# Optimization experiments

Hardware: AMD Instinct MI355X
Metric: run time of the kernel (lower is better)

The kernel has to match this reference:

```python
import jax, jax.numpy as jnp
import numpy as np

B, IN, OUT, LAT = 8192, 256, 256, 128

def setup_inputs() -> dict:
    key = jax.random.key(0)
    ks = jax.random.split(key, 6)
    s = 0.05
    return {
        "x": jax.random.normal(ks[0], (B, IN), dtype=jnp.float32),
        "latent": jax.random.normal(ks[1], (B, LAT), dtype=jnp.float32),
        "Ww": jax.random.normal(ks[2], (LAT, IN * OUT), dtype=jnp.float32) * s,
        "bw": jax.random.normal(ks[3], (IN * OUT,), dtype=jnp.float32) * s,
        "Wb": jax.random.normal(ks[4], (LAT, OUT), dtype=jnp.float32) * s,
        "bb": jax.random.normal(ks[5], (OUT,), dtype=jnp.float32) * s,
    }

def reference(x, latent, Ww, bw, Wb, bb):
    lead = x.shape[:-1]
    x2 = x.reshape(-1, x.shape[-1])            # [B, in]
    l2 = latent.reshape(-1, latent.shape[-1])  # [B, lat]
    # per-sample weight: [B, in, out]
    weight = (l2 @ Ww + bw).reshape(-1, IN, OUT)
    # per-sample bias: [B, out]
    bias = l2 @ Wb + bb
    out = jnp.einsum('bi,bio->bo', x2, weight) + bias
    return out.reshape(*lead, OUT)
```

## Files before the change

### kernel.cpp

```cpp
#include <hip/hip_runtime.h>
#include <cstdint>
#include <cstddef>

#define BATCH  8192
#define IN_N   256
#define OUT_N  256
#define LAT_N  128
#define SLABS  129
#define KT     (SLABS * IN_N)
#define KT16   (KT / 16)
#define SPLITK 4

typedef _Float16 h8 __attribute__((ext_vector_type(8)));
typedef _Float16 h4 __attribute__((ext_vector_type(4)));
typedef _Float16 h2 __attribute__((ext_vector_type(2)));
typedef float    f16v __attribute__((ext_vector_type(16)));
typedef float    f4v  __attribute__((ext_vector_type(4)));

#define AS1 __attribute__((address_space(1)))
#define AS3 __attribute__((address_space(3)))
#define WAITVM0 asm volatile("s_waitcnt vmcnt(0)" ::: "memory")
#define WAITVM2 asm volatile("s_waitcnt vmcnt(2)" ::: "memory")
#define WAITVM3 asm volatile("s_waitcnt vmcnt(3)" ::: "memory")

#define WS_BP    0
#define WS_XH    16908288
#define WS_LT    21102592
#define WS_PARTS 23216128

#define PR_T1   516
#define PR_L1   580
#define PR_X1   1604
#define PR_O1   1608
#define PR_B1   2632
__global__ void k_prep(const float* __restrict__ Ww, const float* __restrict__ bw,
                       const float* __restrict__ x,  const float* __restrict__ latent,
                       const float* __restrict__ Wb, const float* __restrict__ bb,
                       _Float16* __restrict__ Bp, _Float16* __restrict__ Xh,
                       _Float16* __restrict__ LT, float* __restrict__ part0) {
    __shared__ _Float16 smemh[16512];
    const int bid = blockIdx.x;
    const int t   = threadIdx.x;

    if (bid < PR_T1) {
        _Float16* tile = smemh;
        const int k0 = bid * 64;
#pragma unroll
        for (int j = 0; j < 16; ++j) {
            int idx = j * 256 + t;
            int row = idx >> 6, col = (idx & 63) * 4;
            int k = k0 + row;
            const float* src = (k < LAT_N * IN_N)
                             ? Ww + (size_t)k * 256 + col
                             : bw + (size_t)(k - LAT_N * IN_N) * 256 + col;
            float4 v = *(const float4*)src;
            h4 o;
            o[0] = (_Float16)v.x; o[1] = (_Float16)v.y;
            o[2] = (_Float16)v.z; o[3] = (_Float16)v.w;
            *(h4*)(tile + row * 256 + col) = o;
        }
        __syncthreads();
        const int tl = t & 31;
#pragma unroll
        for (int j = 0; j < 4; ++j) {
            int stid = j * 8 + (t >> 5);
            int kt_l = stid >> 3, nt = stid & 7;
            int kt16 = bid * 4 + kt_l;
            _Float16* dst = Bp + ((size_t)(nt * KT16 + kt16) * 64) * 8;
#pragma unroll
            for (int kh = 0; kh < 2; ++kh) {
                h8 v;
#pragma unroll
                for (int h = 0; h < 8; ++h)
                    v[h] = tile[(kt_l * 16 + kh * 8 + h) * 256 + nt * 32 + tl];
                *(h8*)(dst + (size_t)(kh * 32 + tl) * 8) = v;
            }
        }
    } else if (bid < PR_L1) {
        _Float16* t2 = smemh;
        const int b0 = (bid - PR_T1) * 128;
#pragma unroll
        for (int j = 0; j < 16; ++j) {
            int idx = j * 256 + t;
            int b = idx >> 5, l = (idx & 31) * 4;
            float4 v = *(const float4*)(latent + (size_t)(b0 + b) * 128 + l);
            t2[(l + 0) * 129 + b] = (_Float16)v.x;
            t2[(l + 1) * 129 + b] = (_Float16)v.y;
            t2[(l + 2) * 129 + b] = (_Float16)v.z;
            t2[(l + 3) * 129 + b] = (_Float16)v.w;
        }
        __syncthreads();
#pragma unroll
        for (int j = 0; j < 32; ++j) {
            int idx = j * 256 + t;
            int l = idx >> 6, bb2 = (idx & 63) * 2;
            h2 w;
            w[0] = t2[l * 129 + bb2];
            w[1] = t2[l * 129 + bb2 + 1];
            *(h2*)(LT + (size_t)l * BATCH + b0 + bb2) = w;
        }
    } else if (bid < PR_X1) {
        const int cb = bid - PR_L1;
        int i = (cb * 256 + t) * 8;
        float4 v0 = *(const float4*)(x + i);
        float4 v1 = *(const float4*)(x + i + 4);
        h8 o;
        o[0] = (_Float16)v0.x; o[1] = (_Float16)v0.y;
        o[2] = (_Float16)v0.z; o[3] = (_Float16)v0.w;
        o[4] = (_Float16)v1.x; o[5] = (_Float16)v1.y;
        o[6] = (_Float16)v1.z; o[7] = (_Float16)v1.w;
        *(h8*)(Xh + i) = o;
    } else if (bid < PR_O1) {
        const int ob = bid - PR_X1;
        int base = ob * 2048 + t * 8;
        h8 o;
#pragma unroll
        for (int h = 0; h < 8; ++h) o[h] = (_Float16)1.0f;
        *(h8*)(LT + (size_t)LAT_N * BATCH + base) = o;
    } else {
        float* lat = (float*)smemh;
        const int b0 = (bid - PR_O1) * 8;
#pragma unroll
        for (int j = 0; j < 4; ++j) {
            int idx = t + 256 * j;
            int rr = idx >> 7, l = idx & 127;
            lat[rr * 128 + l] = latent[(size_t)(b0 + rr) * 128 + l];
        }
        __syncthreads();
        const int o = t;
        float acc[8];
        float bbv = bb[o];
#pragma unroll
        for (int rr = 0; rr < 8; ++rr) acc[rr] = bbv;
        for (int l = 0; l < 128; ++l) {
            float w = Wb[l * 256 + o];
#pragma unroll
            for (int rr = 0; rr < 8; ++rr) acc[rr] += lat[rr * 128 + l] * w;
        }
#pragma unroll
        for (int rr = 0; rr < 8; ++rr) part0[(size_t)(b0 + rr) * 256 + o] = acc[rr];
    }
}

__global__ __launch_bounds__(512, 2) void k_gemm(const _Float16* __restrict__ Bp,
                                                 const _Float16* __restrict__ Xh,
                                                 const _Float16* __restrict__ LT,
                                                 float* __restrict__ parts) {
    __shared__ __align__(16) _Float16 Bs[4 * 8192];

    const int bid   = blockIdx.x;
    const int ks    = bid & 3;
    const int m_blk = bid >> 2;
    const int m0    = m_blk * 128;
    const int slab0 = (ks == 0) ? 0 : 33 + 32 * (ks - 1);
    const int nslab = (ks == 0) ? 33 : 32;

    const int tid = threadIdx.x, wid = tid >> 6, lane = tid & 63;
    const int l32 = lane & 31, khalf = lane >> 5;
    const int wm = wid >> 1, wn = wid & 1;
    const int wn4 = wn * 4;
    const int mrow = m0 + wm * 32 + l32;

    h8 xv[16];
    const _Float16* xp = Xh + (size_t)mrow * IN_N + khalf * 8;
#pragma unroll
    for (int k = 0; k < 16; ++k) xv[k] = *(const h8*)(xp + k * 16);

    const _Float16* ltp = LT + (size_t)slab0 * BATCH;
    _Float16 s_cur = ltp[mrow];

    const int chunk0 = wid * 2;
    const int ktl0 = chunk0 >> 3, nt0 = chunk0 & 7;
    const char* Bgb = (const char*)Bp;

#define STAGE(bufidx, ktg)                                                                 \
    do {                                                                                   \
        const char* g0_ = Bgb + (((size_t)(nt0 * KT16 + (ktg) + ktl0)) << 10) + (lane << 4);     \
        const char* g1_ = Bgb + (((size_t)((nt0 + 1) * KT16 + (ktg) + ktl0)) << 10) + (lane << 4); \
        _Float16* l0_ = Bs + (bufidx) * 8192 + chunk0 * 512;                               \
        __builtin_amdgcn_global_load_lds((const AS1 void*)g0_, (AS3 void*)l0_, 16, 0, 0);  \
        __builtin_amdgcn_global_load_lds((const AS1 void*)g1_, (AS3 void*)(l0_ + 512), 16, 0, 0); \
    } while (0)

    f16v acc0, acc1, acc2, acc3;
#pragma unroll
    for (int r = 0; r < 16; ++r) { acc0[r] = 0.f; acc1[r] = 0.f; acc2[r] = 0.f; acc3[r] = 0.f; }

#define KSTEP(bufc, sl)                                                                    \
    _Pragma("unroll")                                                                      \
    for (int j = 0; j < 2; ++j) {                                                          \
        const int kx = (((sl) * 2 + j) & 15);                                              \
        h8 a = xv[kx] * s8;                                                                \
        const _Float16* bb = Bs + (bufc) * 8192 + j * 4096 + wn4 * 512 + (lane << 3);      \
        h8 b0 = *(const h8*)(bb);                                                          \
        h8 b1 = *(const h8*)(bb + 512);                                                    \
        h8 b2 = *(const h8*)(bb + 1024);                                                   \
        h8 b3 = *(const h8*)(bb + 1536);                                                   \
        acc0 = __builtin_amdgcn_mfma_f32_32x32x16_f16(a, b0, acc0, 0, 0, 0);               \
        acc1 = __builtin_amdgcn_mfma_f32_32x32x16_f16(a, b1, acc1, 0, 0, 0);               \
        acc2 = __builtin_amdgcn_mfma_f32_32x32x16_f16(a, b2, acc2, 0, 0, 0);               \
        acc3 = __builtin_amdgcn_mfma_f32_32x32x16_f16(a, b3, acc3, 0, 0, 0);               \
    }

    const int kb = slab0 * 16;

    STAGE(0, kb + 0);
    STAGE(1, kb + 2);
    WAITVM2;
    __builtin_amdgcn_s_barrier();
    asm volatile("" ::: "memory");

    for (int s0 = 0; s0 < nslab - 1; ++s0) {
        _Float16 s_nx = ltp[(size_t)(s0 + 1) * BATCH + mrow];
        h8 s8;
#pragma unroll
        for (int h = 0; h < 8; ++h) s8[h] = s_cur;
        const int ktg0 = kb + s0 * 16;
#pragma unroll
        for (int sl = 0; sl < 8; ++sl) {
            STAGE((sl + 2) & 3, ktg0 + (sl + 2) * 2);
            KSTEP(sl & 3, sl);
            if (sl == 0) WAITVM3; else WAITVM2;
            __builtin_amdgcn_s_barrier();
            asm volatile("" ::: "memory");
        }
        s_cur = s_nx;
    }

    {
        h8 s8;
#pragma unroll
        for (int h = 0; h < 8; ++h) s8[h] = s_cur;
        const int ktg0 = kb + (nslab - 1) * 16;
#pragma unroll
        for (int sl = 0; sl < 8; ++sl) {
            if (sl < 6) STAGE((sl + 2) & 3, ktg0 + (sl + 2) * 2);
            KSTEP(sl & 3, sl);
            if (sl < 7) {
                if (sl == 6) WAITVM0; else WAITVM2;
                __builtin_amdgcn_s_barrier();
                asm volatile("" ::: "memory");
            }
        }
    }

    float* dst = parts + (size_t)ks * ((size_t)BATCH * OUT_N);
    const int rowb = m0 + wm * 32;
#define EPI(u, accv)                                                                       \
    {                                                                                      \
        int col = wn * 128 + (u) * 32 + l32;                                               \
        _Pragma("unroll")                                                                  \
        for (int r = 0; r < 16; ++r) {                                                     \
            int row = rowb + (r & 3) + 8 * (r >> 2) + 4 * khalf;                           \
            size_t off = (size_t)row * OUT_N + col;                                        \
            if (ks == 0) dst[off] += accv[r];                                              \
            else         dst[off] = accv[r];                                               \
        }                                                                                  \
    }
    EPI(0, acc0); EPI(1, acc1); EPI(2, acc2); EPI(3, acc3);
#undef EPI
#undef KSTEP
#undef STAGE
}

__global__ void k_reduce(const float* __restrict__ parts, float* __restrict__ out) {
    int i = (blockIdx.x * 256 + threadIdx.x) * 4;
    f4v s = *(const f4v*)(parts + i);
    s += *(const f4v*)(parts + 2097152 + i);
    s += *(const f4v*)(parts + 2 * 2097152 + i);
    s += *(const f4v*)(parts + 3 * 2097152 + i);
    *(f4v*)(out + i) = s;
}

extern "C" void kernel_launch(void* const* d_in, const int* in_sizes, int n_in,
                              void* d_out, int out_size, void* d_ws, size_t ws_size,
                              hipStream_t stream) {
    const float* x      = (const float*)d_in[0];
    const float* latent = (const float*)d_in[1];
    const float* Ww     = (const float*)d_in[2];
    const float* bw     = (const float*)d_in[3];
    const float* Wb     = (const float*)d_in[4];
    const float* bb     = (const float*)d_in[5];

    char* ws = (char*)d_ws;
    _Float16* Bp    = (_Float16*)(ws + WS_BP);
    _Float16* Xh    = (_Float16*)(ws + WS_XH);
    _Float16* LT    = (_Float16*)(ws + WS_LT);
    float*    parts = (float*)(ws + WS_PARTS);
    float*    out   = (float*)d_out;

    k_prep<<<PR_B1, 256, 0, stream>>>(Ww, bw, x, latent, Wb, bb, Bp, Xh, LT, parts);
    k_gemm<<<256, 512, 0, stream>>>(Bp, Xh, LT, parts);
    k_reduce<<<2048, 256, 0, stream>>>(parts, out);
}
```

Before: 252.2 us.

## Retile GEMM warps to 64x64 sub-tiles and drop occupancy hint to one

Changes the per-warp tile from 32 rows x 128 columns to 64 rows x 64 columns (2x2 MFMA blocks). Each warp now loads two B fragments from LDS instead of four per k-step, halving LDS read traffic per MFMA, but it keeps two rows of X in registers (32 h8 vectors) and scales two A operands. Launch bounds drop to one block per CU to make room for the added registers, and the wait count at slab start is adjusted for the extra latent load. The risk is lost occupancy and less latency hiding.

Result: slower. 267.2 us (+6.0%).

```diff
diff --git a/kernel.cpp b/kernel.cpp
--- a/kernel.cpp
+++ b/kernel.cpp
@@ -21,7 +21,7 @@
 #define AS3 __attribute__((address_space(3)))
 #define WAITVM0 asm volatile("s_waitcnt vmcnt(0)" ::: "memory")
 #define WAITVM2 asm volatile("s_waitcnt vmcnt(2)" ::: "memory")
-#define WAITVM3 asm volatile("s_waitcnt vmcnt(3)" ::: "memory")
+#define WAITVM4 asm volatile("s_waitcnt vmcnt(4)" ::: "memory")
 
 #define WS_BP    0
 #define WS_XH    16908288
@@ -142,7 +142,7 @@
     }
 }
 
-__global__ __launch_bounds__(512, 2) void k_gemm(const _Float16* __restrict__ Bp,
+__global__ __launch_bounds__(512, 1) void k_gemm(const _Float16* __restrict__ Bp,
                                                  const _Float16* __restrict__ Xh,
                                                  const _Float16* __restrict__ LT,
                                                  float* __restrict__ parts) {
@@ -157,17 +157,21 @@
 
     const int tid = threadIdx.x, wid = tid >> 6, lane = tid & 63;
     const int l32 = lane & 31, khalf = lane >> 5;
-    const int wm = wid >> 1, wn = wid & 1;
-    const int wn4 = wn * 4;
-    const int mrow = m0 + wm * 32 + l32;
-
-    h8 xv[16];
-    const _Float16* xp = Xh + (size_t)mrow * IN_N + khalf * 8;
-#pragma unroll
-    for (int k = 0; k < 16; ++k) xv[k] = *(const h8*)(xp + k * 16);
+    const int wm = wid >> 2, wn = wid & 3;
+    const int mrow0 = m0 + wm * 64 + l32;
+    const int mrow1 = mrow0 + 32;
+
+    h8 xv0[16], xv1[16];
+    const _Float16* xp0 = Xh + (size_t)mrow0 * IN_N + khalf * 8;
+    const _Float16* xp1 = Xh + (size_t)mrow1 * IN_N + khalf * 8;
+#pragma unroll
+    for (int k = 0; k < 16; ++k) {
+        xv0[k] = *(const h8*)(xp0 + k * 16);
+        xv1[k] = *(const h8*)(xp1 + k * 16);
+    }
 
     const _Float16* ltp = LT + (size_t)slab0 * BATCH;
-    _Float16 s_cur = ltp[mrow];
+    _Float16 sc0 = ltp[mrow0], sc1 = ltp[mrow1];
 
     const int chunk0 = wid * 2;
     const int ktl0 = chunk0 >> 3, nt0 = chunk0 & 7;
@@ -182,24 +186,23 @@
         __builtin_amdgcn_global_load_lds((const AS1 void*)g1_, (AS3 void*)(l0_ + 512), 16, 0, 0); \
     } while (0)
 
-    f16v acc0, acc1, acc2, acc3;
-#pragma unroll
-    for (int r = 0; r < 16; ++r) { acc0[r] = 0.f; acc1[r] = 0.f; acc2[r] = 0.f; acc3[r] = 0.f; }
+    f16v acc00, acc01, acc10, acc11;
+#pragma unroll
+    for (int r = 0; r < 16; ++r) { acc00[r] = 0.f; acc01[r] = 0.f; acc10[r] = 0.f; acc11[r] = 0.f; }
 
 #define KSTEP(bufc, sl)                                                                    \
     _Pragma("unroll")                                                                      \
     for (int j = 0; j < 2; ++j) {                                                          \
         const int kx = (((sl) * 2 + j) & 15);                                              \
-        h8 a = xv[kx] * s8;                                                                \
-        const _Float16* bb = Bs + (bufc) * 8192 + j * 4096 + wn4 * 512 + (lane << 3);      \
+        h8 a0 = xv0[kx] * s80;                                                             \
+        h8 a1 = xv1[kx] * s81;                                                             \
+        const _Float16* bb = Bs + (bufc) * 8192 + j * 4096 + wn * 1024 + (lane << 3);      \
         h8 b0 = *(const h8*)(bb);                                                          \
         h8 b1 = *(const h8*)(bb + 512);                                                    \
-        h8 b2 = *(const h8*)(bb + 1024);                                                   \
-        h8 b3 = *(const h8*)(bb + 1536);                                                   \
-        acc0 = __builtin_amdgcn_mfma_f32_32x32x16_f16(a, b0, acc0, 0, 0, 0);               \
-        acc1 = __builtin_amdgcn_mfma_f32_32x32x16_f16(a, b1, acc1, 0, 0, 0);               \
-        acc2 = __builtin_amdgcn_mfma_f32_32x32x16_f16(a, b2, acc2, 0, 0, 0);               \
-        acc3 = __builtin_amdgcn_mfma_f32_32x32x16_f16(a, b3, acc3, 0, 0, 0);               \
+        acc00 = __builtin_amdgcn_mfma_f32_32x32x16_f16(a0, b0, acc00, 0, 0, 0);            \
+        acc01 = __builtin_amdgcn_mfma_f32_32x32x16_f16(a0, b1, acc01, 0, 0, 0);            \
+        acc10 = __builtin_amdgcn_mfma_f32_32x32x16_f16(a1, b0, acc10, 0, 0, 0);            \
+        acc11 = __builtin_amdgcn_mfma_f32_32x32x16_f16(a1, b1, acc11, 0, 0, 0);            \
     }
 
     const int kb = slab0 * 16;
@@ -211,26 +214,27 @@
     asm volatile("" ::: "memory");
 
     for (int s0 = 0; s0 < nslab - 1; ++s0) {
-        _Float16 s_nx = ltp[(size_t)(s0 + 1) * BATCH + mrow];
-        h8 s8;
-#pragma unroll
-        for (int h = 0; h < 8; ++h) s8[h] = s_cur;
+        _Float16 sn0 = ltp[(size_t)(s0 + 1) * BATCH + mrow0];
+        _Float16 sn1 = ltp[(size_t)(s0 + 1) * BATCH + mrow1];
+        h8 s80, s81;
+#pragma unroll
+        for (int h = 0; h < 8; ++h) { s80[h] = sc0; s81[h] = sc1; }
         const int ktg0 = kb + s0 * 16;
 #pragma unroll
         for (int sl = 0; sl < 8; ++sl) {
             STAGE((sl + 2) & 3, ktg0 + (sl + 2) * 2);
             KSTEP(sl & 3, sl);
-            if (sl == 0) WAITVM3; else WAITVM2;
+            if (sl == 0) WAITVM4; else WAITVM2;
             __builtin_amdgcn_s_barrier();
             asm volatile("" ::: "memory");
         }
-        s_cur = s_nx;
+        sc0 = sn0; sc1 = sn1;
     }
 
     {
-        h8 s8;
-#pragma unroll
-        for (int h = 0; h < 8; ++h) s8[h] = s_cur;
+        h8 s80, s81;
+#pragma unroll
+        for (int h = 0; h < 8; ++h) { s80[h] = sc0; s81[h] = sc1; }
         const int ktg0 = kb + (nslab - 1) * 16;
 #pragma unroll
         for (int sl = 0; sl < 8; ++sl) {
@@ -245,19 +249,20 @@
     }
 
     float* dst = parts + (size_t)ks * ((size_t)BATCH * OUT_N);
-    const int rowb = m0 + wm * 32;
-#define EPI(u, accv)                                                                       \
+    const int rowb0 = m0 + wm * 64;
+#define EPI(rowb, u, accv)                                                                 \
     {                                                                                      \
-        int col = wn * 128 + (u) * 32 + l32;                                               \
+        int col = wn * 64 + (u) * 32 + l32;                                                \
         _Pragma("unroll")                                                                  \
         for (int r = 0; r < 16; ++r) {                                                     \
-            int row = rowb + (r & 3) + 8 * (r >> 2) + 4 * khalf;                           \
+            int row = (rowb) + (r & 3) + 8 * (r >> 2) + 4 * khalf;                         \
             size_t off = (size_t)row * OUT_N + col;                                        \
             if (ks == 0) dst[off] += accv[r];                                              \
             else         dst[off] = accv[r];                                               \
         }                                                                                  \
     }
-    EPI(0, acc0); EPI(1, acc1); EPI(2, acc2); EPI(3, acc3);
+    EPI(rowb0,      0, acc00); EPI(rowb0,      1, acc01);
+    EPI(rowb0 + 32, 0, acc10); EPI(rowb0 + 32, 1, acc11);
 #undef EPI
 #undef KSTEP
 #undef STAGE
```
